# Kernel tuning notes

Hardware: AMD Instinct MI355X
Metric: run time of the kernel (lower is better)

## Reference

```python
import jax, jax.numpy as jnp
import numpy as np

B, S, D = 2, 2048, 768
E, TOP_K = 8, 2
H = 4 * D  # expert hidden dim


def setup_inputs() -> dict:
    key = jax.random.key(0)
    ks = jax.random.split(key, 8)
    s_in = 1.0 / np.sqrt(D)
    s_h = 1.0 / np.sqrt(H)
    return {
        "x": jax.random.normal(ks[0], (B, S, D), dtype=jnp.float32),
        "gate_w": jax.random.uniform(ks[1], (D, E), jnp.float32, -s_in, s_in),
        "gate_b": jax.random.uniform(ks[2], (E,), jnp.float32, -s_in, s_in),
        "w1": jax.random.uniform(ks[3], (E, D, H), jnp.float32, -s_in, s_in),
        "b1": jax.random.uniform(ks[4], (E, H), jnp.float32, -s_in, s_in),
        "w2": jax.random.uniform(ks[5], (E, H, D), jnp.float32, -s_h, s_h),
        "b2": jax.random.uniform(ks[6], (E, D), jnp.float32, -s_h, s_h),
    }


def reference(x, gate_w, gate_b, w1, b1, w2, b2):
    # Router: gate linear -> top-k -> softmax over the k selected logits
    logits = jnp.einsum("bsd,de->bse", x, gate_w) + gate_b          # [B,S,E]
    top_vals, top_idx = jax.lax.top_k(logits, TOP_K)                 # [B,S,K]
    rw = jax.nn.softmax(top_vals, axis=-1)                           # [B,S,K]
    # Per-token per-expert combine weight (0 for unselected experts)
    onehot = jax.nn.one_hot(top_idx, E, dtype=x.dtype)               # [B,S,K,E]
    expert_w = jnp.einsum("bske,bsk->bse", onehot, rw)               # [B,S,E]

    # Expert MLPs (GELU exact, matching torch nn.GELU default; dropout is
    # identity in eval). Stacked as grouped GEMMs over the expert axis.
    h = jax.nn.gelu(jnp.einsum("bsd,edh->bseh", x, w1) + b1, approximate=False)
    y = jnp.einsum("bseh,ehd->bsed", h, w2) + b2                     # [B,S,E,D]
    # Weighted combine over experts
    return jnp.einsum("bse,bsed->bsd", expert_w, y)                  # [B,S,D]
```

## Files before the change

kernel.cpp:

```cpp
#include <hip/hip_runtime.h>
#include <hip/hip_bf16.h>

#define D_ 768
#define E_ 8
#define H_ 3072
#define N_TOK 4096
#define BT 64
#define BK 64

typedef _Float16 f16;
typedef f16 f16x8 __attribute__((ext_vector_type(8)));
typedef float f32x4 __attribute__((ext_vector_type(4)));

__device__ __forceinline__ void gld16(const f16* g, f16* l) {
    __builtin_amdgcn_global_load_lds(
        (const __attribute__((address_space(1))) unsigned int*)g,
        (__attribute__((address_space(3))) unsigned int*)l, 16, 0, 0);
}

__device__ __forceinline__ int prefix_off(const int* counts, int e, int* cnt_out) {
    int off = 0, cnt = 0;
#pragma unroll
    for (int q = 0; q < E_; q++) {
        int cq = counts[q];
        if (q < e) off += cq;
        if (q == e) cnt = cq;
    }
    *cnt_out = cnt;
    return off;
}

__global__ __launch_bounds__(256) void cvt_w_both(const float* __restrict__ w1,
                                                  const float* __restrict__ w2,
                                                  f16* __restrict__ w1t,
                                                  f16* __restrict__ w2t) {
    __shared__ f16 t[64][66];
    int z = blockIdx.z;
    const float* src; f16* dst; int R, C, xb, yb;
    int bx = blockIdx.x;
    if (z < E_) {
        src = w1 + (size_t)z * D_ * H_; dst = w1t + (size_t)z * D_ * H_;
        R = D_; C = H_; xb = bx % 48; yb = bx / 48;
    } else {
        src = w2 + (size_t)(z - E_) * H_ * D_; dst = w2t + (size_t)(z - E_) * H_ * D_;
        R = H_; C = D_; xb = bx % 12; yb = bx / 12;
    }
    int r0 = yb * 64, c0 = xb * 64;
    int tid = threadIdx.x;
    {
        int r = tid >> 4;
        int c = (tid & 15) * 4;
#pragma unroll
        for (int i = 0; i < 4; i++) {
            float4 v = *(const float4*)(src + (size_t)(r0 + r + i * 16) * C + (c0 + c));
            t[r + i * 16][c] = (f16)v.x;
            t[r + i * 16][c + 1] = (f16)v.y;
            t[r + i * 16][c + 2] = (f16)v.z;
            t[r + i * 16][c + 3] = (f16)v.w;
        }
    }
    __syncthreads();
    {
        int c = tid >> 3;
        int rr = (tid & 7) * 8;
        int ch = rr >> 3;
#pragma unroll
        for (int i = 0; i < 2; i++) {
            int cc = c + i * 32;
            int rowi = c0 + cc;
            f16x8 o;
#pragma unroll
            for (int j = 0; j < 8; j++) o[j] = t[rr + j][cc];
            *(f16x8*)(dst + (size_t)rowi * R + r0 + (((ch ^ rowi) & 7) << 3)) = o;
        }
    }
}

__global__ __launch_bounds__(1024) void router(const float* __restrict__ x,
                                               const float* __restrict__ gw,
                                               const float* __restrict__ gb,
                                               int* __restrict__ counts,
                                               int* __restrict__ list,
                                               float* __restrict__ wslot) {
    __shared__ int lcount[E_];
    __shared__ int lbase[E_];
    __shared__ int te0[64], te1[64], ts0[64], ts1[64];
    __shared__ float tw0[64], tw1[64];

    int tid = threadIdx.x;
    int wv = tid >> 6, lane = tid & 63;
    int s = lane >> 3, eL = lane & 7;
    if (tid < E_) lcount[tid] = 0;
    __syncthreads();

    float biasL = gb[eL];

#pragma unroll 1
    for (int i = 0; i < 4; i++) {
        int lt = wv * 4 + i;
        int tok = blockIdx.x * 64 + lt;
        const float* xr = x + (size_t)tok * D_;
        float a = 0.f;
        const float* gwl = gw + lane;
#pragma unroll 8
        for (int j = 0; j < 96; j++)
            a = fmaf(xr[j * 8 + s], gwl[j * 64], a);
        a += __shfl_xor(a, 8, 64);
        a += __shfl_xor(a, 16, 64);
        a += __shfl_xor(a, 32, 64);
        float lg = a + biasL;
        float le[8];
#pragma unroll
        for (int q = 0; q < 8; q++) le[q] = __shfl(lg, q, 64);
        float v0 = -3.4e38f, v1 = -3.4e38f;
        int i0 = 0, i1 = 0;
#pragma unroll
        for (int q = 0; q < 8; q++) {
            float l = le[q];
            if (l > v0) { v1 = v0; i1 = i0; v0 = l; i0 = q; }
            else if (l > v1) { v1 = l; i1 = q; }
        }
        if (lane == 0) {
            float p1 = expf(v1 - v0);
            float ssum = 1.f + p1;
            int s0 = atomicAdd(&lcount[i0], 1);
            int s1 = atomicAdd(&lcount[i1], 1);
            te0[lt] = i0; ts0[lt] = s0; tw0[lt] = 1.f / ssum;
            te1[lt] = i1; ts1[lt] = s1; tw1[lt] = p1 / ssum;
        }
    }
    __syncthreads();
    if (tid < E_) lbase[tid] = atomicAdd(&counts[tid], lcount[tid]);
    __syncthreads();
    if (tid < 64) {
        int tok = blockIdx.x * 64 + tid;
        int e0 = te0[tid], e1 = te1[tid];
        list[e0 * N_TOK + lbase[e0] + ts0[tid]] = tok * 2;
        list[e1 * N_TOK + lbase[e1] + ts1[tid]] = tok * 2 + 1;
        wslot[tok * 2] = tw0[tid];
        wslot[tok * 2 + 1] = tw1[tid];
    }
}

__global__ __launch_bounds__(256) void pack_a(const float* __restrict__ x,
                                              const int* __restrict__ counts,
                                              const int* __restrict__ list,
                                              f16* __restrict__ xg) {
    int wv = threadIdx.x >> 6, lane = threadIdx.x & 63;
    int idx = blockIdx.x * 4 + wv;
    int e = idx >> 12, j = idx & (N_TOK - 1);
    int cnt;
    int off = prefix_off(counts, e, &cnt);
    if (j >= cnt) return;
    int id = list[idx];
    int row = off + j;
    const float* xr = x + (size_t)(id >> 1) * D_;
    f16* dst = xg + (size_t)row * D_;
    int r7 = row & 7;
#pragma unroll
    for (int c = 0; c < 3; c++) {
        int h = lane * 4 + c * 256;
        float4 v = *(const float4*)(xr + h);
        f16 o[4] = {(f16)v.x, (f16)v.y, (f16)v.z, (f16)v.w};
        int hs = (h & ~0x3F) | ((((h >> 3) ^ r7) & 7) << 3) | (h & 7);
        *(float2*)(dst + hs) = *(const float2*)o;
    }
}

__global__ __launch_bounds__(256, 8) void gemm1(const f16* __restrict__ xg,
                                                const f16* __restrict__ w1t,
                                                const float* __restrict__ b1,
                                                const int* __restrict__ counts,
                                                f16* __restrict__ hbuf) {
    int bid = blockIdx.x;
    int e = bid & 7;
    int r = bid >> 3;
    int xb24 = r % 24;
    int yb = (r / 24) % 64;
    int xh = r / (24 * 64);
    int cnt;
    int off = prefix_off(counts, e, &cnt);
    int rb = yb * BT;
    if (rb >= cnt) return;
    int cb = (xh * 24 + xb24) * BT;

    __shared__ f16 lds[2 * BT * BK];
    char* ldsb = (char*)lds;

    int tid = threadIdx.x;
    int wv = tid >> 6, lane = tid & 63;
    int lr = lane >> 3, lc = lane & 7;

    int r0l = wv * 8 + lr;
    int r1l = 32 + wv * 8 + lr;
    int ag0 = off + rb + r0l; if (ag0 > 8191) ag0 = 8191;
    int ag1 = off + rb + r1l; if (ag1 > 8191) ag1 = 8191;
    const f16* ap0 = xg + (size_t)ag0 * D_ + lc * 8;
    const f16* ap1 = xg + (size_t)ag1 * D_ + lc * 8;
    const f16* wb = w1t + (size_t)e * H_ * D_;
    const f16* bp0 = wb + (size_t)(cb + r0l) * D_ + lc * 8;
    const f16* bp1 = wb + (size_t)(cb + r1l) * D_ + lc * 8;
    f16* la0 = lds + wv * 512;
    f16* la1 = lds + 2048 + wv * 512;
    f16* lb0 = lds + 4096 + wv * 512;
    f16* lb1 = lds + 6144 + wv * 512;

    int wr = (wv >> 1) * 32, wc = (wv & 1) * 32;
    int fr = lane & 15, qh = lane >> 4;
    int koff = (off + rb) & 7;

    int roA[2][2], roB[2][2];
#pragma unroll
    for (int m = 0; m < 2; m++)
#pragma unroll
        for (int ks = 0; ks < 2; ks++) {
            int row = wr + m * 16 + fr;
            roA[m][ks] = row * 128 + ((((ks * 4 + qh) ^ (koff + row)) & 7) << 4);
            int rwb = wc + m * 16 + fr;
            roB[m][ks] = 8192 + rwb * 128 + ((((ks * 4 + qh) ^ rwb) & 7) << 4);
        }

    f32x4 acc[2][2] = {};
    const int NT = D_ / BK;
#pragma unroll 1
    for (int t = 0; t < NT; ++t) {
        int kk = t * BK;
        gld16(ap0 + kk, la0);
        gld16(ap1 + kk, la1);
        gld16(bp0 + kk, lb0);
        gld16(bp1 + kk, lb1);
        __syncthreads();
#pragma unroll
        for (int ks = 0; ks < 2; ks++) {
            f16x8 a0 = *(const f16x8*)(ldsb + roA[0][ks]);
            f16x8 a1 = *(const f16x8*)(ldsb + roA[1][ks]);
            f16x8 b0 = *(const f16x8*)(ldsb + roB[0][ks]);
            f16x8 b1v = *(const f16x8*)(ldsb + roB[1][ks]);
            acc[0][0] = __builtin_amdgcn_mfma_f32_16x16x32_f16(a0, b0, acc[0][0], 0, 0, 0);
            acc[0][1] = __builtin_amdgcn_mfma_f32_16x16x32_f16(a0, b1v, acc[0][1], 0, 0, 0);
            acc[1][0] = __builtin_amdgcn_mfma_f32_16x16x32_f16(a1, b0, acc[1][0], 0, 0, 0);
            acc[1][1] = __builtin_amdgcn_mfma_f32_16x16x32_f16(a1, b1v, acc[1][1], 0, 0, 0);
        }
        __syncthreads();
    }

#pragma unroll
    for (int n = 0; n < 2; n++) {
        int colg = cb + wc + n * 16 + fr;
        float bias = b1[e * H_ + colg];
#pragma unroll
        for (int m = 0; m < 2; m++) {
#pragma unroll
            for (int r2 = 0; r2 < 4; r2++) {
                int j = rb + wr + m * 16 + qh * 4 + r2;
                if (j < cnt) {
                    float v = acc[m][n][r2] + bias;
                    v = 0.5f * v * (1.f + erff(v * 0.70710678f));
                    int row = off + j;
                    int hs = (colg & ~0x3F) | ((((colg >> 3) ^ row) & 7) << 3) | (colg & 7);
                    hbuf[(size_t)row * H_ + hs] = (f16)v;
                }
            }
        }
    }
}

#define KSPLIT 2
#define KCH (H_ / KSPLIT)
__global__ __launch_bounds__(256, 8) void gemm2(const f16* __restrict__ hbuf,
                                                const f16* __restrict__ w2t,
                                                const float* __restrict__ b2,
                                                const int* __restrict__ counts,
                                                const int* __restrict__ list,
                                                const float* __restrict__ wslot,
                                                float* __restrict__ out) {
    int bid = blockIdx.x;
    int e = bid & 7;
    int r = bid >> 3;
    int cb12 = r % 12;
    int yb = (r / 12) % 64;
    int kz = r / (12 * 64);
    int cnt;
    int off = prefix_off(counts, e, &cnt);
    int rb = yb * BT;
    if (rb >= cnt) return;
    int cb = cb12 * BT;
    int k0 = kz * KCH;

    __shared__ f16 lds[2 * BT * BK];
    char* ldsb = (char*)lds;

    int tid = threadIdx.x;
    int wv = tid >> 6, lane = tid & 63;
    int lr = lane >> 3, lc = lane & 7;

    int r0l = wv * 8 + lr;
    int r1l = 32 + wv * 8 + lr;
    int ag0 = off + rb + r0l; if (ag0 > 8191) ag0 = 8191;
    int ag1 = off + rb + r1l; if (ag1 > 8191) ag1 = 8191;
    const f16* ap0 = hbuf + (size_t)ag0 * H_ + k0 + lc * 8;
    const f16* ap1 = hbuf + (size_t)ag1 * H_ + k0 + lc * 8;
    const f16* wb = w2t + (size_t)e * D_ * H_;
    const f16* bp0 = wb + (size_t)(cb + r0l) * H_ + k0 + lc * 8;
    const f16* bp1 = wb + (size_t)(cb + r1l) * H_ + k0 + lc * 8;
    f16* la0 = lds + wv * 512;
    f16* la1 = lds + 2048 + wv * 512;
    f16* lb0 = lds + 4096 + wv * 512;
    f16* lb1 = lds + 6144 + wv * 512;

    int wr = (wv >> 1) * 32, wc = (wv & 1) * 32;
    int fr = lane & 15, qh = lane >> 4;
    int koff = (off + rb) & 7;

    int roA[2][2], roB[2][2];
#pragma unroll
    for (int m = 0; m < 2; m++)
#pragma unroll
        for (int ks = 0; ks < 2; ks++) {
            int row = wr + m * 16 + fr;
            roA[m][ks] = row * 128 + ((((ks * 4 + qh) ^ (koff + row)) & 7) << 4);
            int rwb = wc + m * 16 + fr;
            roB[m][ks] = 8192 + rwb * 128 + ((((ks * 4 + qh) ^ rwb) & 7) << 4);
        }

    f32x4 acc[2][2] = {};
    const int NT = KCH / BK;
#pragma unroll 1
    for (int t = 0; t < NT; ++t) {
        int kk = t * BK;
        gld16(ap0 + kk, la0);
        gld16(ap1 + kk, la1);
        gld16(bp0 + kk, lb0);
        gld16(bp1 + kk, lb1);
        __syncthreads();
#pragma unroll
        for (int ks = 0; ks < 2; ks++) {
            f16x8 a0 = *(const f16x8*)(ldsb + roA[0][ks]);
            f16x8 a1 = *(const f16x8*)(ldsb + roA[1][ks]);
            f16x8 b0 = *(const f16x8*)(ldsb + roB[0][ks]);
            f16x8 b1v = *(const f16x8*)(ldsb + roB[1][ks]);
            acc[0][0] = __builtin_amdgcn_mfma_f32_16x16x32_f16(a0, b0, acc[0][0], 0, 0, 0);
            acc[0][1] = __builtin_amdgcn_mfma_f32_16x16x32_f16(a0, b1v, acc[0][1], 0, 0, 0);
            acc[1][0] = __builtin_amdgcn_mfma_f32_16x16x32_f16(a1, b0, acc[1][0], 0, 0, 0);
            acc[1][1] = __builtin_amdgcn_mfma_f32_16x16x32_f16(a1, b1v, acc[1][1], 0, 0, 0);
        }
        __syncthreads();
    }

#pragma unroll
    for (int n = 0; n < 2; n++) {
        int colg = cb + wc + n * 16 + fr;
        float bias = (kz == 0) ? b2[e * D_ + colg] : 0.f;
#pragma unroll
        for (int m = 0; m < 2; m++) {
#pragma unroll
            for (int r2 = 0; r2 < 4; r2++) {
                int j = rb + wr + m * 16 + qh * 4 + r2;
                if (j < cnt) {
                    int id = list[e * N_TOK + j];
                    float w = wslot[id];
                    float v = (acc[m][n][r2] + bias) * w;
                    atomicAdd(&out[(size_t)(id >> 1) * D_ + colg], v);
                }
            }
        }
    }
}

extern "C" void kernel_launch(void* const* d_in, const int* in_sizes, int n_in,
                              void* d_out, int out_size, void* d_ws, size_t ws_size,
                              hipStream_t stream) {
    const float* x = (const float*)d_in[0];
    const float* gate_w = (const float*)d_in[1];
    const float* gate_b = (const float*)d_in[2];
    const float* w1 = (const float*)d_in[3];
    const float* b1 = (const float*)d_in[4];
    const float* w2 = (const float*)d_in[5];
    const float* b2 = (const float*)d_in[6];
    float* out = (float*)d_out;

    char* ws = (char*)d_ws;
    int* counts = (int*)ws;
    int* list = (int*)(ws + 1024);
    float* wslot = (float*)(ws + 132096);
    f16* xg = (f16*)(ws + 196608);
    f16* w1t = (f16*)(ws + 12779520);
    f16* w2t = (f16*)(ws + 50528256);
    f16* hbuf = (f16*)(ws + 88276992);

    hipMemsetAsync(counts, 0, 256, stream);
    hipMemsetAsync(out, 0, (size_t)out_size * sizeof(float), stream);

    router<<<64, 1024, 0, stream>>>(x, gate_w, gate_b, counts, list, wslot);
    pack_a<<<E_ * N_TOK / 4, 256, 0, stream>>>(x, counts, list, xg);
    cvt_w_both<<<dim3(576, 1, 16), 256, 0, stream>>>(w1, w2, w1t, w2t);
    gemm1<<<E_ * 2 * 64 * 24, 256, 0, stream>>>(xg, w1t, b1, counts, hbuf);
    gemm2<<<E_ * 2 * 64 * 12, 256, 0, stream>>>(hbuf, w2t, b2, counts, list, wslot, out);
}
```

Measured before the change: 252.8 us.

## Merge weight conversion and token packing into one launch; drop gemm2 K-split

Weight fp32-to-fp16 transpose and gathered-token packing now run in a single prep kernel, with block index choosing the role. This removes one launch and lets the two independent jobs overlap on the GPU. gemm2 no longer splits the 3072-long reduction into two halves, so each block does the full K loop and issues half as many atomic adds to the output. The cost is half as many gemm2 blocks and twice the serial K work per block, which may underfill the device for small expert groups.

Result: faster. 238.4 us (median of 2 runs) (-5.7%).

```diff
diff --git a/kernel.cpp b/kernel.cpp
--- a/kernel.cpp
+++ b/kernel.cpp
@@ -28,52 +28,6 @@
     }
     *cnt_out = cnt;
     return off;
-}
-
-__global__ __launch_bounds__(256) void cvt_w_both(const float* __restrict__ w1,
-                                                  const float* __restrict__ w2,
-                                                  f16* __restrict__ w1t,
-                                                  f16* __restrict__ w2t) {
-    __shared__ f16 t[64][66];
-    int z = blockIdx.z;
-    const float* src; f16* dst; int R, C, xb, yb;
-    int bx = blockIdx.x;
-    if (z < E_) {
-        src = w1 + (size_t)z * D_ * H_; dst = w1t + (size_t)z * D_ * H_;
-        R = D_; C = H_; xb = bx % 48; yb = bx / 48;
-    } else {
-        src = w2 + (size_t)(z - E_) * H_ * D_; dst = w2t + (size_t)(z - E_) * H_ * D_;
-        R = H_; C = D_; xb = bx % 12; yb = bx / 12;
-    }
-    int r0 = yb * 64, c0 = xb * 64;
-    int tid = threadIdx.x;
-    {
-        int r = tid >> 4;
-        int c = (tid & 15) * 4;
-#pragma unroll
-        for (int i = 0; i < 4; i++) {
-            float4 v = *(const float4*)(src + (size_t)(r0 + r + i * 16) * C + (c0 + c));
-            t[r + i * 16][c] = (f16)v.x;
-            t[r + i * 16][c + 1] = (f16)v.y;
-            t[r + i * 16][c + 2] = (f16)v.z;
-            t[r + i * 16][c + 3] = (f16)v.w;
-        }
-    }
-    __syncthreads();
-    {
-        int c = tid >> 3;
-        int rr = (tid & 7) * 8;
-        int ch = rr >> 3;
-#pragma unroll
-        for (int i = 0; i < 2; i++) {
-            int cc = c + i * 32;
-            int rowi = c0 + cc;
-            f16x8 o;
-#pragma unroll
-            for (int j = 0; j < 8; j++) o[j] = t[rr + j][cc];
-            *(f16x8*)(dst + (size_t)rowi * R + r0 + (((ch ^ rowi) & 7) << 3)) = o;
-        }
-    }
 }
 
 __global__ __launch_bounds__(1024) void router(const float* __restrict__ x,
@@ -142,28 +96,78 @@
     }
 }
 
-__global__ __launch_bounds__(256) void pack_a(const float* __restrict__ x,
-                                              const int* __restrict__ counts,
-                                              const int* __restrict__ list,
-                                              f16* __restrict__ xg) {
-    int wv = threadIdx.x >> 6, lane = threadIdx.x & 63;
-    int idx = blockIdx.x * 4 + wv;
-    int e = idx >> 12, j = idx & (N_TOK - 1);
-    int cnt;
-    int off = prefix_off(counts, e, &cnt);
-    if (j >= cnt) return;
-    int id = list[idx];
-    int row = off + j;
-    const float* xr = x + (size_t)(id >> 1) * D_;
-    f16* dst = xg + (size_t)row * D_;
-    int r7 = row & 7;
-#pragma unroll
-    for (int c = 0; c < 3; c++) {
-        int h = lane * 4 + c * 256;
-        float4 v = *(const float4*)(xr + h);
-        f16 o[4] = {(f16)v.x, (f16)v.y, (f16)v.z, (f16)v.w};
-        int hs = (h & ~0x3F) | ((((h >> 3) ^ r7) & 7) << 3) | (h & 7);
-        *(float2*)(dst + hs) = *(const float2*)o;
+#define CVT_BLKS 9216
+__global__ __launch_bounds__(256) void prep(const float* __restrict__ w1,
+                                            const float* __restrict__ w2,
+                                            f16* __restrict__ w1t,
+                                            f16* __restrict__ w2t,
+                                            const float* __restrict__ x,
+                                            const int* __restrict__ counts,
+                                            const int* __restrict__ list,
+                                            f16* __restrict__ xg) {
+    __shared__ f16 t[64][66];
+    int bid = blockIdx.x;
+    int tid = threadIdx.x;
+
+    if (bid < CVT_BLKS) {
+        int z = bid / 576;
+        int bx = bid % 576;
+        const float* src; f16* dst; int R, C, xb, yb;
+        if (z < E_) {
+            src = w1 + (size_t)z * D_ * H_; dst = w1t + (size_t)z * D_ * H_;
+            R = D_; C = H_; xb = bx % 48; yb = bx / 48;
+        } else {
+            src = w2 + (size_t)(z - E_) * H_ * D_; dst = w2t + (size_t)(z - E_) * H_ * D_;
+            R = H_; C = D_; xb = bx % 12; yb = bx / 12;
+        }
+        int r0 = yb * 64, c0 = xb * 64;
+        {
+            int r = tid >> 4;
+            int c = (tid & 15) * 4;
+#pragma unroll
+            for (int i = 0; i < 4; i++) {
+                float4 v = *(const float4*)(src + (size_t)(r0 + r + i * 16) * C + (c0 + c));
+                t[r + i * 16][c] = (f16)v.x;
+                t[r + i * 16][c + 1] = (f16)v.y;
+                t[r + i * 16][c + 2] = (f16)v.z;
+                t[r + i * 16][c + 3] = (f16)v.w;
+            }
+        }
+        __syncthreads();
+        {
+            int c = tid >> 3;
+            int rr = (tid & 7) * 8;
+            int ch = rr >> 3;
+#pragma unroll
+            for (int i = 0; i < 2; i++) {
+                int cc = c + i * 32;
+                int rowi = c0 + cc;
+                f16x8 o;
+#pragma unroll
+                for (int j = 0; j < 8; j++) o[j] = t[rr + j][cc];
+                *(f16x8*)(dst + (size_t)rowi * R + r0 + (((ch ^ rowi) & 7) << 3)) = o;
+            }
+        }
+    } else {
+        int wv = tid >> 6, lane = tid & 63;
+        int idx = (bid - CVT_BLKS) * 4 + wv;
+        int e = idx >> 12, j = idx & (N_TOK - 1);
+        int cnt;
+        int off = prefix_off(counts, e, &cnt);
+        if (j >= cnt) return;
+        int id = list[idx];
+        int row = off + j;
+        const float* xr = x + (size_t)(id >> 1) * D_;
+        f16* dst = xg + (size_t)row * D_;
+        int r7 = row & 7;
+#pragma unroll
+        for (int c = 0; c < 3; c++) {
+            int h = lane * 4 + c * 256;
+            float4 v = *(const float4*)(xr + h);
+            f16 o[4] = {(f16)v.x, (f16)v.y, (f16)v.z, (f16)v.w};
+            int hs = (h & ~0x3F) | ((((h >> 3) ^ r7) & 7) << 3) | (h & 7);
+            *(float2*)(dst + hs) = *(const float2*)o;
+        }
     }
 }
 
@@ -265,8 +269,6 @@
     }
 }
 
-#define KSPLIT 2
-#define KCH (H_ / KSPLIT)
 __global__ __launch_bounds__(256, 8) void gemm2(const f16* __restrict__ hbuf,
                                                 const f16* __restrict__ w2t,
                                                 const float* __restrict__ b2,
@@ -278,14 +280,12 @@
     int e = bid & 7;
     int r = bid >> 3;
     int cb12 = r % 12;
-    int yb = (r / 12) % 64;
-    int kz = r / (12 * 64);
+    int yb = r / 12;
     int cnt;
     int off = prefix_off(counts, e, &cnt);
     int rb = yb * BT;
     if (rb >= cnt) return;
     int cb = cb12 * BT;
-    int k0 = kz * KCH;
 
     __shared__ f16 lds[2 * BT * BK];
     char* ldsb = (char*)lds;
@@ -298,11 +298,11 @@
     int r1l = 32 + wv * 8 + lr;
     int ag0 = off + rb + r0l; if (ag0 > 8191) ag0 = 8191;
     int ag1 = off + rb + r1l; if (ag1 > 8191) ag1 = 8191;
-    const f16* ap0 = hbuf + (size_t)ag0 * H_ + k0 + lc * 8;
-    const f16* ap1 = hbuf + (size_t)ag1 * H_ + k0 + lc * 8;
+    const f16* ap0 = hbuf + (size_t)ag0 * H_ + lc * 8;
+    const f16* ap1 = hbuf + (size_t)ag1 * H_ + lc * 8;
     const f16* wb = w2t + (size_t)e * D_ * H_;
-    const f16* bp0 = wb + (size_t)(cb + r0l) * H_ + k0 + lc * 8;
-    const f16* bp1 = wb + (size_t)(cb + r1l) * H_ + k0 + lc * 8;
+    const f16* bp0 = wb + (size_t)(cb + r0l) * H_ + lc * 8;
+    const f16* bp1 = wb + (size_t)(cb + r1l) * H_ + lc * 8;
     f16* la0 = lds + wv * 512;
     f16* la1 = lds + 2048 + wv * 512;
     f16* lb0 = lds + 4096 + wv * 512;
@@ -324,7 +324,7 @@
         }
 
     f32x4 acc[2][2] = {};
-    const int NT = KCH / BK;
+    const int NT = H_ / BK;
 #pragma unroll 1
     for (int t = 0; t < NT; ++t) {
         int kk = t * BK;
@@ -350,7 +350,7 @@
 #pragma unroll
     for (int n = 0; n < 2; n++) {
         int colg = cb + wc + n * 16 + fr;
-        float bias = (kz == 0) ? b2[e * D_ + colg] : 0.f;
+        float bias = b2[e * D_ + colg];
 #pragma unroll
         for (int m = 0; m < 2; m++) {
 #pragma unroll
@@ -392,8 +392,7 @@
     hipMemsetAsync(out, 0, (size_t)out_size * sizeof(float), stream);
 
     router<<<64, 1024, 0, stream>>>(x, gate_w, gate_b, counts, list, wslot);
-    pack_a<<<E_ * N_TOK / 4, 256, 0, stream>>>(x, counts, list, xg);
-    cvt_w_both<<<dim3(576, 1, 16), 256, 0, stream>>>(w1, w2, w1t, w2t);
+    prep<<<CVT_BLKS + E_ * N_TOK / 4, 256, 0, stream>>>(w1, w2, w1t, w2t, x, counts, list, xg);
     gemm1<<<E_ * 2 * 64 * 24, 256, 0, stream>>>(xg, w1t, b1, counts, hbuf);
-    gemm2<<<E_ * 2 * 64 * 12, 256, 0, stream>>>(hbuf, w2t, b2, counts, list, wslot, out);
-}
+    gemm2<<<E_ * 64 * 12, 256, 0, stream>>>(hbuf, w2t, b2, counts, list, wslot, out);
+}
```
